# Optimization experiments

Measured on AMD Instinct MI355X. Metric: run time of the kernel, lower is better.

Reference implementation:

```python
import jax, jax.numpy as jnp
import numpy as np

EOS_IDX = 2


def setup_inputs() -> dict:
    key = jax.random.key(0)
    k1, k2 = jax.random.split(key)
    B, S, D = 64, 2048, 1024
    feature = jax.random.normal(k1, (B, S, D), dtype=jnp.float32)
    input_ids = jax.random.randint(k2, (B, S), 3, 33, dtype=jnp.int64)
    # guarantee every row has an eos (last column), like real tokenized sequences
    input_ids = input_ids.at[:, S - 1].set(EOS_IDX)
    return {"feature": feature, "input_ids": input_ids}


def reference(feature, input_ids):
    # MEAN pooling: for each row i, mean over feature[i, 1:last_eos_i, :]
    B, S, D = feature.shape
    pos = jnp.arange(S)
    eq = input_ids == EOS_IDX                       # [B, S]
    # last eos position; 0 if none (matches torch zeros init)
    last_eos = jnp.max(jnp.where(eq, pos[None, :], 0), axis=1)  # [B]
    # mask positions j with 1 <= j < last_eos_i
    mask = ((pos[None, :] >= 1) & (pos[None, :] < last_eos[:, None])).astype(feature.dtype)  # [B, S]
    summed = jnp.einsum("bsd,bs->bd", feature, mask)            # [B, D]
    counts = jnp.sum(mask, axis=1, keepdims=True)               # [B, 1]
    return summed / counts
```

## Files before the change

kernel.cpp:

```cpp
#include <hip/hip_runtime.h>

#define EOS_IDX 2
#define NSPLIT 32

typedef float v4f __attribute__((ext_vector_type(4)));

__device__ __forceinline__ int row_last_eos(const int* __restrict__ row, int S) {
    int m = 0;
    for (int j = threadIdx.x; j < S; j += blockDim.x) {
        if (row[j] == EOS_IDX) m = max(m, j);
    }
    #pragma unroll
    for (int off = 32; off > 0; off >>= 1) m = max(m, __shfl_xor(m, off, 64));
    __shared__ int sm[8];
    const int wid = threadIdx.x >> 6;
    const int nw  = blockDim.x >> 6;
    if ((threadIdx.x & 63) == 0) sm[wid] = m;
    __syncthreads();
    int r = sm[0];
    for (int w = 1; w < nw; ++w) r = max(r, sm[w]);
    return r;
}

__global__ __launch_bounds__(256) void pool_kernel(const float* __restrict__ feat,
                                                   const int* __restrict__ ids,
                                                   float* __restrict__ partial,
                                                   int S, int D, int jchunk) {
    const int b  = blockIdx.x;
    const int le = row_last_eos(ids + (size_t)b * S, S);

    const int j0 = blockIdx.y * jchunk;
    const int lo = max(j0, 1);
    const int hi = min(j0 + jchunk, le);

    const int d4n = D >> 2;
    const v4f* base = (const v4f*)(feat + (size_t)b * S * D);
    v4f* pout = (v4f*)(partial + ((size_t)b * NSPLIT + blockIdx.y) * D);

    for (int d4 = threadIdx.x; d4 < d4n; d4 += blockDim.x) {
        v4f s0 = {0.f, 0.f, 0.f, 0.f};
        v4f s1 = s0, s2 = s0, s3 = s0;
        int j = lo;
        for (; j + 4 <= hi; j += 4) {
            v4f a0 = __builtin_nontemporal_load(base + (size_t)(j + 0) * d4n + d4);
            v4f a1 = __builtin_nontemporal_load(base + (size_t)(j + 1) * d4n + d4);
            v4f a2 = __builtin_nontemporal_load(base + (size_t)(j + 2) * d4n + d4);
            v4f a3 = __builtin_nontemporal_load(base + (size_t)(j + 3) * d4n + d4);
            s0 += a0; s1 += a1; s2 += a2; s3 += a3;
        }
        for (; j < hi; ++j)
            s0 += __builtin_nontemporal_load(base + (size_t)j * d4n + d4);
        pout[d4] = (s0 + s1) + (s2 + s3);
    }
}

__global__ __launch_bounds__(256) void reduce_kernel(const float* __restrict__ partial,
                                                     const int* __restrict__ ids,
                                                     float* __restrict__ out,
                                                     int S, int D) {
    const int b  = blockIdx.x;
    const int le = row_last_eos(ids + (size_t)b * S, S);
    const float inv = 1.0f / (float)(le - 1);

    const int d = blockIdx.y * blockDim.x + threadIdx.x;
    if (d < D) {
        const float* p = partial + (size_t)b * NSPLIT * D + d;
        float s = 0.f;
        #pragma unroll
        for (int t = 0; t < NSPLIT; ++t) s += p[(size_t)t * D];
        out[(size_t)b * D + d] = s * inv;
    }
}

extern "C" void kernel_launch(void* const* d_in, const int* in_sizes, int n_in,
                              void* d_out, int out_size, void* d_ws, size_t ws_size,
                              hipStream_t stream) {
    const float* feat = (const float*)d_in[0];
    const int*   ids  = (const int*)d_in[1];

    const int BS = in_sizes[1];
    const int D  = in_sizes[0] / BS;
    const int B  = out_size / D;
    const int S  = BS / B;

    float* partial = (float*)d_ws;

    const int jchunk = (S + NSPLIT - 1) / NSPLIT;
    dim3 pgrid(B, NSPLIT);
    pool_kernel<<<pgrid, 256, 0, stream>>>(feat, ids, partial, S, D, jchunk);

    dim3 rgrid(B, (D + 255) / 256);
    reduce_kernel<<<rgrid, 256, 0, stream>>>(partial, ids, (float*)d_out, S, D);
}
```

Baseline: 98.02 us.

## Halve split count, unroll pool loop by eight, move scaling into pool kernel

Cuts the sequence split from 32 to 16 chunks per row and unrolls the accumulation loop to eight independent loads and accumulators, so each thread has more memory requests in flight. The 1/count scaling now happens in the pool kernel, which lets the reduce kernel drop its own EOS scan over the ids and do a vectorized float4 sum in one block per row. The trade-off is fewer blocks (1024 instead of 2048) in the bandwidth-bound pool kernel and higher register use.

```diff
diff --git a/kernel.cpp b/kernel.cpp
--- a/kernel.cpp
+++ b/kernel.cpp
@@ -1,7 +1,7 @@
 #include <hip/hip_runtime.h>
 
 #define EOS_IDX 2
-#define NSPLIT 32
+#define NSPLIT 16
 
 typedef float v4f __attribute__((ext_vector_type(4)));
 
@@ -28,6 +28,7 @@
                                                    int S, int D, int jchunk) {
     const int b  = blockIdx.x;
     const int le = row_last_eos(ids + (size_t)b * S, S);
+    const float inv = 1.0f / (float)(le - 1);
 
     const int j0 = blockIdx.y * jchunk;
     const int lo = max(j0, 1);
@@ -39,36 +40,39 @@
 
     for (int d4 = threadIdx.x; d4 < d4n; d4 += blockDim.x) {
         v4f s0 = {0.f, 0.f, 0.f, 0.f};
-        v4f s1 = s0, s2 = s0, s3 = s0;
+        v4f s1 = s0, s2 = s0, s3 = s0, s4 = s0, s5 = s0, s6 = s0, s7 = s0;
         int j = lo;
-        for (; j + 4 <= hi; j += 4) {
-            v4f a0 = __builtin_nontemporal_load(base + (size_t)(j + 0) * d4n + d4);
-            v4f a1 = __builtin_nontemporal_load(base + (size_t)(j + 1) * d4n + d4);
-            v4f a2 = __builtin_nontemporal_load(base + (size_t)(j + 2) * d4n + d4);
-            v4f a3 = __builtin_nontemporal_load(base + (size_t)(j + 3) * d4n + d4);
+        for (; j + 8 <= hi; j += 8) {
+            const v4f* p = base + (size_t)j * d4n + d4;
+            v4f a0 = __builtin_nontemporal_load(p + 0 * d4n);
+            v4f a1 = __builtin_nontemporal_load(p + 1 * d4n);
+            v4f a2 = __builtin_nontemporal_load(p + 2 * d4n);
+            v4f a3 = __builtin_nontemporal_load(p + 3 * d4n);
+            v4f a4 = __builtin_nontemporal_load(p + 4 * d4n);
+            v4f a5 = __builtin_nontemporal_load(p + 5 * d4n);
+            v4f a6 = __builtin_nontemporal_load(p + 6 * d4n);
+            v4f a7 = __builtin_nontemporal_load(p + 7 * d4n);
             s0 += a0; s1 += a1; s2 += a2; s3 += a3;
+            s4 += a4; s5 += a5; s6 += a6; s7 += a7;
         }
         for (; j < hi; ++j)
             s0 += __builtin_nontemporal_load(base + (size_t)j * d4n + d4);
-        pout[d4] = (s0 + s1) + (s2 + s3);
+        v4f t = ((s0 + s1) + (s2 + s3)) + ((s4 + s5) + (s6 + s7));
+        pout[d4] = t * inv;
     }
 }
 
 __global__ __launch_bounds__(256) void reduce_kernel(const float* __restrict__ partial,
-                                                     const int* __restrict__ ids,
-                                                     float* __restrict__ out,
-                                                     int S, int D) {
-    const int b  = blockIdx.x;
-    const int le = row_last_eos(ids + (size_t)b * S, S);
-    const float inv = 1.0f / (float)(le - 1);
-
-    const int d = blockIdx.y * blockDim.x + threadIdx.x;
-    if (d < D) {
-        const float* p = partial + (size_t)b * NSPLIT * D + d;
-        float s = 0.f;
+                                                     float* __restrict__ out, int D) {
+    const int b   = blockIdx.x;
+    const int d4n = D >> 2;
+    const v4f* p  = (const v4f*)(partial + (size_t)b * NSPLIT * D);
+    v4f* o        = (v4f*)(out + (size_t)b * D);
+    for (int d4 = threadIdx.x; d4 < d4n; d4 += blockDim.x) {
+        v4f s = {0.f, 0.f, 0.f, 0.f};
         #pragma unroll
-        for (int t = 0; t < NSPLIT; ++t) s += p[(size_t)t * D];
-        out[(size_t)b * D + d] = s * inv;
+        for (int t = 0; t < NSPLIT; ++t) s += p[(size_t)t * d4n + d4];
+        o[d4] = s;
     }
 }
 
@@ -89,6 +93,5 @@
     dim3 pgrid(B, NSPLIT);
     pool_kernel<<<pgrid, 256, 0, stream>>>(feat, ids, partial, S, D, jchunk);
 
-    dim3 rgrid(B, (D + 255) / 256);
-    reduce_kernel<<<rgrid, 256, 0, stream>>>(partial, ids, (float*)d_out, S, D);
+    reduce_kernel<<<B, 256, 0, stream>>>(partial, (float*)d_out, D);
 }
```

New measurement: 89.60 us. 8.6% less time.
